# Kernel optimization log

Measured on AMD Instinct MI355X. Metric: run time of the kernel, lower is better.

## Reference

```python
import jax, jax.numpy as jnp
import numpy as np

TS = 0.01  # Euler step size (module's `ts`)

N_X, N_U, N_FEAT = 32, 16, 512
BATCH, SEQ_LEN = 512, 2048


def setup_inputs() -> dict:
    key = jax.random.key(0)
    k0, k1, k2, k3 = jax.random.split(key, 4)
    x0_batch = jax.random.normal(k0, (BATCH, 1, N_X), dtype=jnp.float32)
    u_batch = jax.random.normal(k1, (BATCH, SEQ_LEN, N_U), dtype=jnp.float32)
    # 2-layer MLP state-space model: Linear(n_x+n_u, n_feat) -> Tanh -> Linear(n_feat, n_x)
    fan1 = N_X + N_U
    W1 = jax.random.normal(k2, (fan1, N_FEAT), dtype=jnp.float32) / np.sqrt(fan1).astype(np.float32)
    b1 = jnp.zeros((N_FEAT,), dtype=jnp.float32)
    W2 = jax.random.normal(k3, (N_FEAT, N_X), dtype=jnp.float32) / np.sqrt(N_FEAT).astype(np.float32)
    b2 = jnp.zeros((N_X,), dtype=jnp.float32)
    return {"x0_batch": x0_batch, "u_batch": u_batch, "W1": W1, "b1": b1, "W2": W2, "b2": b2}


def reference(x0_batch, u_batch, W1, b1, W2, b2):
    # x0_batch: (B, 1, n_x); u_batch: (B, T, n_u) -> out: (B, T, n_x)
    x0 = x0_batch[:, 0, :]                       # (B, n_x)
    u_t = jnp.swapaxes(u_batch, 0, 1)            # (T, B, n_u) for scan over time

    def step(x, u):
        h = jnp.tanh(jnp.concatenate([x, u], axis=-1) @ W1 + b1)  # (B, n_feat)
        dx = h @ W2 + b2                                           # (B, n_x)
        x_next = x + TS * dx
        return x_next, x_next

    _, xs = jax.lax.scan(step, x0, u_t)          # xs: (T, B, n_x)
    return jnp.swapaxes(xs, 0, 1)                # (B, T, n_x)
```

## Files before the change

### kernel.cpp

```cpp
#include <hip/hip_runtime.h>

constexpr int NX = 32, NU = 16, NF = 512;
constexpr int SEQ = 2048;
constexpr int CH = 32;
constexpr int NT = 256;
constexpr float SC = 2.88539008177792681f;

template<int CTRL>
__device__ __forceinline__ float dpp_add(float v) {
    int t = __builtin_amdgcn_update_dpp(0, __float_as_int(v), CTRL, 0xF, 0xF, true);
    return v + __int_as_float(t);
}

__device__ __forceinline__ float tanh4(float y) {
    const float e = __builtin_amdgcn_exp2f(y);
    const float r = __builtin_amdgcn_rcpf(e + 1.f);
    return fmaf(-2.f, r, 1.f);
}

__global__ __launch_bounds__(NT, 2)
void fes_kernel(const float* __restrict__ x0, const float* __restrict__ ug,
                const float* __restrict__ W1, const float* __restrict__ b1,
                const float* __restrict__ W2, const float* __restrict__ b2,
                float* __restrict__ out)
{
    __shared__ float4 xs4[NX / 4];
    __shared__ float4 hs4[NF / 4];
    __shared__ float4 us4[CH * NU / 4];

    const int tid = threadIdx.x, row = blockIdx.x;
    const int g   = tid >> 1, kh = tid & 1;
    const int sl  = tid >> 4, l  = tid & 15;
    const int j0  = sl, j1 = sl + 16;

    float w1r[96];
#pragma unroll
    for (int i = 0; i < 24; ++i)
#pragma unroll
        for (int c = 0; c < 4; ++c)
            w1r[i * 4 + c] = SC * W1[(kh * 24 + i) * NF + 4 * g + c];
    float b1s[4];
#pragma unroll
    for (int c = 0; c < 4; ++c) b1s[c] = kh ? 0.f : SC * b1[4 * g + c];

    float w2a[32], w2b[32];
#pragma unroll
    for (int i = 0; i < 8; ++i)
#pragma unroll
        for (int c = 0; c < 4; ++c) {
            const int f = 4 * (l + 16 * i) + c;
            w2a[4 * i + c] = 0.01f * W2[f * NX + j0];
            w2b[4 * i + c] = 0.01f * W2[f * NX + j1];
        }
    const float bb0 = 0.01f * b2[j0], bb1 = 0.01f * b2[j1];

    float xr0 = x0[row * NX + j0];
    float xr1 = x0[row * NX + j1];

    const float* ug_row  = ug  + (size_t)row * SEQ * NU;
    float*       out_row = out + (size_t)row * SEQ * NX;

    if (tid < NX / 4) xs4[tid] = ((const float4*)(x0 + row * NX))[tid];

    const float4* bA = kh ? xs4 + 6 : xs4;

    for (int t0 = 0; t0 < SEQ; t0 += CH) {
        if (tid < CH * NU / 4)
            us4[tid] = *(const float4*)&ug_row[(size_t)t0 * NU + tid * 4];
        __syncthreads();

#pragma unroll 1
        for (int tc = 0; tc < CH; ++tc) {
            const int t = t0 + tc;
            const float4* bB = kh ? us4 + tc * 4 - 2 : xs4;
            const float4 iv0 = bA[0], iv1 = bA[1];
            const float4 iv2 = bB[2], iv3 = bB[3], iv4 = bB[4], iv5 = bB[5];
            float a0 = b1s[0], a1 = b1s[1], a2 = b1s[2], a3 = b1s[3];
#define G1F4(iv, q)                                                        \
            a0 = fmaf(w1r[(q)*16 + 0],  iv.x, a0);                         \
            a1 = fmaf(w1r[(q)*16 + 1],  iv.x, a1);                         \
            a2 = fmaf(w1r[(q)*16 + 2],  iv.x, a2);                         \
            a3 = fmaf(w1r[(q)*16 + 3],  iv.x, a3);                         \
            a0 = fmaf(w1r[(q)*16 + 4],  iv.y, a0);                         \
            a1 = fmaf(w1r[(q)*16 + 5],  iv.y, a1);                         \
            a2 = fmaf(w1r[(q)*16 + 6],  iv.y, a2);                         \
            a3 = fmaf(w1r[(q)*16 + 7],  iv.y, a3);                         \
            a0 = fmaf(w1r[(q)*16 + 8],  iv.z, a0);                         \
            a1 = fmaf(w1r[(q)*16 + 9],  iv.z, a1);                         \
            a2 = fmaf(w1r[(q)*16 + 10], iv.z, a2);                         \
            a3 = fmaf(w1r[(q)*16 + 11], iv.z, a3);                         \
            a0 = fmaf(w1r[(q)*16 + 12], iv.w, a0);                         \
            a1 = fmaf(w1r[(q)*16 + 13], iv.w, a1);                         \
            a2 = fmaf(w1r[(q)*16 + 14], iv.w, a2);                         \
            a3 = fmaf(w1r[(q)*16 + 15], iv.w, a3);
            G1F4(iv0, 0) G1F4(iv1, 1) G1F4(iv2, 2)
            G1F4(iv3, 3) G1F4(iv4, 4) G1F4(iv5, 5)
#undef G1F4
            a0 = dpp_add<0xB1>(a0);
            a1 = dpp_add<0xB1>(a1);
            a2 = dpp_add<0xB1>(a2);
            a3 = dpp_add<0xB1>(a3);
            float2 hw;
            hw.x = tanh4(kh ? a2 : a0);
            hw.y = tanh4(kh ? a3 : a1);
            ((float2*)hs4)[g * 2 + kh] = hw;
            __syncthreads();

            float sa0 = 0.f, sa1 = 0.f, sa2 = 0.f, sa3 = 0.f;
            float sb0 = 0.f, sb1 = 0.f, sb2 = 0.f, sb3 = 0.f;
#pragma unroll
            for (int i = 0; i < 8; ++i) {
                const float4 hv = hs4[l + 16 * i];
                sa0 = fmaf(hv.x, w2a[4*i],   sa0);
                sa1 = fmaf(hv.y, w2a[4*i+1], sa1);
                sa2 = fmaf(hv.z, w2a[4*i+2], sa2);
                sa3 = fmaf(hv.w, w2a[4*i+3], sa3);
                sb0 = fmaf(hv.x, w2b[4*i],   sb0);
                sb1 = fmaf(hv.y, w2b[4*i+1], sb1);
                sb2 = fmaf(hv.z, w2b[4*i+2], sb2);
                sb3 = fmaf(hv.w, w2b[4*i+3], sb3);
            }
            float sa = (sa0 + sa1) + (sa2 + sa3);
            float sb = (sb0 + sb1) + (sb2 + sb3);
            sa = dpp_add<0xB1>(sa);   sb = dpp_add<0xB1>(sb);
            sa = dpp_add<0x4E>(sa);   sb = dpp_add<0x4E>(sb);
            sa = dpp_add<0x124>(sa);  sb = dpp_add<0x124>(sb);
            sa = dpp_add<0x128>(sa);  sb = dpp_add<0x128>(sb);

            const float xn0 = xr0 + (sa + bb0);
            const float xn1 = xr1 + (sb + bb1);
            xr0 = xn0; xr1 = xn1;
            if (l < 2) {
                const float v  = l ? xn1 : xn0;
                const int   jj = j0 + (l << 4);
                ((float*)xs4)[jj] = v;
                out_row[(size_t)t * NX + jj] = v;
            }
            __syncthreads();
        }
    }
}

extern "C" void kernel_launch(void* const* d_in, const int* in_sizes, int n_in,
                              void* d_out, int out_size, void* d_ws, size_t ws_size,
                              hipStream_t stream) {
    const float* x0 = (const float*)d_in[0];
    const float* ug = (const float*)d_in[1];
    const float* W1 = (const float*)d_in[2];
    const float* b1 = (const float*)d_in[3];
    const float* W2 = (const float*)d_in[4];
    const float* b2 = (const float*)d_in[5];
    float* out = (float*)d_out;

    fes_kernel<<<dim3(512), dim3(NT), 0, stream>>>(x0, ug, W1, b1, W2, b2, out);
}
```

Baseline: 1.747 ms.

## Use packed FMA and reorganize output-stage reduction across 32-lane groups

Both matvecs are rewritten to use two-wide packed FP32 FMAs (v2f), which may compile to v_pk_fma_f32 and halve FMA instruction count. The second-layer work is remapped so each 32-lane half-wave reduces four output states over 512 features via a five-step DPP tree. One owner lane then writes a float4 to shared memory and global output instead of two scalar stores. This raises register use for packed weights and lengthens the reduction chain, at the risk of extra latency on the serial critical path.

```diff
diff --git a/kernel.cpp b/kernel.cpp
--- a/kernel.cpp
+++ b/kernel.cpp
@@ -1,4 +1,6 @@
 #include <hip/hip_runtime.h>
+
+typedef float v2f __attribute__((ext_vector_type(2)));
 
 constexpr int NX = 32, NU = 16, NF = 512;
 constexpr int SEQ = 2048;
@@ -18,6 +20,8 @@
     return fmaf(-2.f, r, 1.f);
 }
 
+__device__ __forceinline__ v2f pkfma(v2f a, v2f b, v2f c) { return a * b + c; }
+
 __global__ __launch_bounds__(NT, 2)
 void fes_kernel(const float* __restrict__ x0, const float* __restrict__ ug,
                 const float* __restrict__ W1, const float* __restrict__ b1,
@@ -29,33 +33,39 @@
     __shared__ float4 us4[CH * NU / 4];
 
     const int tid = threadIdx.x, row = blockIdx.x;
-    const int g   = tid >> 1, kh = tid & 1;
-    const int sl  = tid >> 4, l  = tid & 15;
-    const int j0  = sl, j1 = sl + 16;
+    const int lam = tid & 63, w = tid >> 6;
+    const int g = tid >> 1, kh = tid & 1;
+    const int sk = (lam & 15) | (((lam >> 4) & 1) << 4);
+    const int os = ((lam >> 5) & 1) + 2 * w;
+    const bool owner = (lam & 31) == 31;
 
-    float w1r[96];
+    v2f wk[48];
 #pragma unroll
-    for (int i = 0; i < 24; ++i)
+    for (int i = 0; i < 4; ++i)
 #pragma unroll
-        for (int c = 0; c < 4; ++c)
-            w1r[i * 4 + c] = SC * W1[(kh * 24 + i) * NF + 4 * g + c];
-    float b1s[4];
+        for (int kp = 0; kp < 12; ++kp) {
+            const int k = 24 * kh + 2 * kp;
+            wk[i * 12 + kp] = v2f{SC * W1[k * NF + 4 * g + i],
+                                  SC * W1[(k + 1) * NF + 4 * g + i]};
+        }
+    const float b1e = SC * b1[4 * g + 2 * kh];
+    const float b1o = SC * b1[4 * g + 2 * kh + 1];
+
+    v2f wc[4][8];
 #pragma unroll
-    for (int c = 0; c < 4; ++c) b1s[c] = kh ? 0.f : SC * b1[4 * g + c];
-
-    float w2a[32], w2b[32];
+    for (int c = 0; c < 4; ++c)
 #pragma unroll
-    for (int i = 0; i < 8; ++i)
+        for (int m = 0; m < 4; ++m)
 #pragma unroll
-        for (int c = 0; c < 4; ++c) {
-            const int f = 4 * (l + 16 * i) + c;
-            w2a[4 * i + c] = 0.01f * W2[f * NX + j0];
-            w2b[4 * i + c] = 0.01f * W2[f * NX + j1];
-        }
-    const float bb0 = 0.01f * b2[j0], bb1 = 0.01f * b2[j1];
-
-    float xr0 = x0[row * NX + j0];
-    float xr1 = x0[row * NX + j1];
+            for (int p = 0; p < 2; ++p) {
+                const int k = 128 * m + 4 * sk + 2 * p;
+                wc[c][2 * m + p] = v2f{0.01f * W2[k * NX + 4 * os + c],
+                                       0.01f * W2[(k + 1) * NX + 4 * os + c]};
+            }
+    float bb0 = 0.01f * b2[4 * os + 0], bb1 = 0.01f * b2[4 * os + 1];
+    float bb2 = 0.01f * b2[4 * os + 2], bb3 = 0.01f * b2[4 * os + 3];
+    float xr0 = x0[row * NX + 4 * os + 0], xr1 = x0[row * NX + 4 * os + 1];
+    float xr2 = x0[row * NX + 4 * os + 2], xr3 = x0[row * NX + 4 * os + 3];
 
     const float* ug_row  = ug  + (size_t)row * SEQ * NU;
     float*       out_row = out + (size_t)row * SEQ * NX;
@@ -63,6 +73,7 @@
     if (tid < NX / 4) xs4[tid] = ((const float4*)(x0 + row * NX))[tid];
 
     const float4* bA = kh ? xs4 + 6 : xs4;
+    const float4* hp = hs4 + sk;
 
     for (int t0 = 0; t0 < SEQ; t0 += CH) {
         if (tid < CH * NU / 4)
@@ -72,69 +83,69 @@
 #pragma unroll 1
         for (int tc = 0; tc < CH; ++tc) {
             const int t = t0 + tc;
-            const float4* bB = kh ? us4 + tc * 4 - 2 : xs4;
+            const float4* bB = kh ? us4 + 4 * tc - 2 : xs4;
             const float4 iv0 = bA[0], iv1 = bA[1];
             const float4 iv2 = bB[2], iv3 = bB[3], iv4 = bB[4], iv5 = bB[5];
-            float a0 = b1s[0], a1 = b1s[1], a2 = b1s[2], a3 = b1s[3];
-#define G1F4(iv, q)                                                        \
-            a0 = fmaf(w1r[(q)*16 + 0],  iv.x, a0);                         \
-            a1 = fmaf(w1r[(q)*16 + 1],  iv.x, a1);                         \
-            a2 = fmaf(w1r[(q)*16 + 2],  iv.x, a2);                         \
-            a3 = fmaf(w1r[(q)*16 + 3],  iv.x, a3);                         \
-            a0 = fmaf(w1r[(q)*16 + 4],  iv.y, a0);                         \
-            a1 = fmaf(w1r[(q)*16 + 5],  iv.y, a1);                         \
-            a2 = fmaf(w1r[(q)*16 + 6],  iv.y, a2);                         \
-            a3 = fmaf(w1r[(q)*16 + 7],  iv.y, a3);                         \
-            a0 = fmaf(w1r[(q)*16 + 8],  iv.z, a0);                         \
-            a1 = fmaf(w1r[(q)*16 + 9],  iv.z, a1);                         \
-            a2 = fmaf(w1r[(q)*16 + 10], iv.z, a2);                         \
-            a3 = fmaf(w1r[(q)*16 + 11], iv.z, a3);                         \
-            a0 = fmaf(w1r[(q)*16 + 12], iv.w, a0);                         \
-            a1 = fmaf(w1r[(q)*16 + 13], iv.w, a1);                         \
-            a2 = fmaf(w1r[(q)*16 + 14], iv.w, a2);                         \
-            a3 = fmaf(w1r[(q)*16 + 15], iv.w, a3);
-            G1F4(iv0, 0) G1F4(iv1, 1) G1F4(iv2, 2)
-            G1F4(iv3, 3) G1F4(iv4, 4) G1F4(iv5, 5)
-#undef G1F4
-            a0 = dpp_add<0xB1>(a0);
-            a1 = dpp_add<0xB1>(a1);
-            a2 = dpp_add<0xB1>(a2);
-            a3 = dpp_add<0xB1>(a3);
+            v2f a0 = {0.f, 0.f}, a1 = {0.f, 0.f}, a2 = {0.f, 0.f}, a3 = {0.f, 0.f};
+#define G1S(iv, s)                                                          \
+            {   const v2f lo = {iv.x, iv.y}, hi = {iv.z, iv.w};             \
+                a0 = pkfma(wk[0*12 + 2*(s)], lo, a0);                       \
+                a1 = pkfma(wk[1*12 + 2*(s)], lo, a1);                       \
+                a2 = pkfma(wk[2*12 + 2*(s)], lo, a2);                       \
+                a3 = pkfma(wk[3*12 + 2*(s)], lo, a3);                       \
+                a0 = pkfma(wk[0*12 + 2*(s) + 1], hi, a0);                   \
+                a1 = pkfma(wk[1*12 + 2*(s) + 1], hi, a1);                   \
+                a2 = pkfma(wk[2*12 + 2*(s) + 1], hi, a2);                   \
+                a3 = pkfma(wk[3*12 + 2*(s) + 1], hi, a3); }
+            G1S(iv0, 0) G1S(iv1, 1) G1S(iv2, 2) G1S(iv3, 3) G1S(iv4, 4) G1S(iv5, 5)
+#undef G1S
+            float h0 = a0.x + a0.y, h1 = a1.x + a1.y;
+            float h2 = a2.x + a2.y, h3 = a3.x + a3.y;
+            h0 = dpp_add<0xB1>(h0);  h1 = dpp_add<0xB1>(h1);
+            h2 = dpp_add<0xB1>(h2);  h3 = dpp_add<0xB1>(h3);
+            const float he = kh ? h2 : h0, ho = kh ? h3 : h1;
             float2 hw;
-            hw.x = tanh4(kh ? a2 : a0);
-            hw.y = tanh4(kh ? a3 : a1);
-            ((float2*)hs4)[g * 2 + kh] = hw;
+            hw.x = tanh4(he + b1e);
+            hw.y = tanh4(ho + b1o);
+            ((float2*)hs4)[2 * g + kh] = hw;
             __syncthreads();
 
-            float sa0 = 0.f, sa1 = 0.f, sa2 = 0.f, sa3 = 0.f;
-            float sb0 = 0.f, sb1 = 0.f, sb2 = 0.f, sb3 = 0.f;
+            v2f A0 = {0.f, 0.f}, A1 = {0.f, 0.f}, A2 = {0.f, 0.f}, A3 = {0.f, 0.f};
 #pragma unroll
-            for (int i = 0; i < 8; ++i) {
-                const float4 hv = hs4[l + 16 * i];
-                sa0 = fmaf(hv.x, w2a[4*i],   sa0);
-                sa1 = fmaf(hv.y, w2a[4*i+1], sa1);
-                sa2 = fmaf(hv.z, w2a[4*i+2], sa2);
-                sa3 = fmaf(hv.w, w2a[4*i+3], sa3);
-                sb0 = fmaf(hv.x, w2b[4*i],   sb0);
-                sb1 = fmaf(hv.y, w2b[4*i+1], sb1);
-                sb2 = fmaf(hv.z, w2b[4*i+2], sb2);
-                sb3 = fmaf(hv.w, w2b[4*i+3], sb3);
+            for (int m = 0; m < 4; ++m) {
+                const float4 hv = hp[32 * m];
+                const v2f lo = {hv.x, hv.y}, hi = {hv.z, hv.w};
+                A0 = pkfma(wc[0][2 * m], lo, A0);
+                A1 = pkfma(wc[1][2 * m], lo, A1);
+                A2 = pkfma(wc[2][2 * m], lo, A2);
+                A3 = pkfma(wc[3][2 * m], lo, A3);
+                A0 = pkfma(wc[0][2 * m + 1], hi, A0);
+                A1 = pkfma(wc[1][2 * m + 1], hi, A1);
+                A2 = pkfma(wc[2][2 * m + 1], hi, A2);
+                A3 = pkfma(wc[3][2 * m + 1], hi, A3);
             }
-            float sa = (sa0 + sa1) + (sa2 + sa3);
-            float sb = (sb0 + sb1) + (sb2 + sb3);
-            sa = dpp_add<0xB1>(sa);   sb = dpp_add<0xB1>(sb);
-            sa = dpp_add<0x4E>(sa);   sb = dpp_add<0x4E>(sb);
-            sa = dpp_add<0x124>(sa);  sb = dpp_add<0x124>(sb);
-            sa = dpp_add<0x128>(sa);  sb = dpp_add<0x128>(sb);
+            float s0 = A0.x + A0.y, s1 = A1.x + A1.y;
+            float s2 = A2.x + A2.y, s3 = A3.x + A3.y;
+            s0 = dpp_add<0xB1>(s0);  s1 = dpp_add<0xB1>(s1);
+            s2 = dpp_add<0xB1>(s2);  s3 = dpp_add<0xB1>(s3);
+            s0 = dpp_add<0x4E>(s0);  s1 = dpp_add<0x4E>(s1);
+            s2 = dpp_add<0x4E>(s2);  s3 = dpp_add<0x4E>(s3);
+            s0 = dpp_add<0x124>(s0); s1 = dpp_add<0x124>(s1);
+            s2 = dpp_add<0x124>(s2); s3 = dpp_add<0x124>(s3);
+            s0 = dpp_add<0x128>(s0); s1 = dpp_add<0x128>(s1);
+            s2 = dpp_add<0x128>(s2); s3 = dpp_add<0x128>(s3);
+            s0 = dpp_add<0x142>(s0); s1 = dpp_add<0x142>(s1);
+            s2 = dpp_add<0x142>(s2); s3 = dpp_add<0x142>(s3);
 
-            const float xn0 = xr0 + (sa + bb0);
-            const float xn1 = xr1 + (sb + bb1);
-            xr0 = xn0; xr1 = xn1;
-            if (l < 2) {
-                const float v  = l ? xn1 : xn0;
-                const int   jj = j0 + (l << 4);
-                ((float*)xs4)[jj] = v;
-                out_row[(size_t)t * NX + jj] = v;
+            const float xn0 = xr0 + (s0 + bb0);
+            const float xn1 = xr1 + (s1 + bb1);
+            const float xn2 = xr2 + (s2 + bb2);
+            const float xn3 = xr3 + (s3 + bb3);
+            xr0 = xn0; xr1 = xn1; xr2 = xn2; xr3 = xn3;
+            if (owner) {
+                const float4 xv = {xn0, xn1, xn2, xn3};
+                xs4[os] = xv;
+                *(float4*)&out_row[(size_t)t * NX + 4 * os] = xv;
             }
             __syncthreads();
         }
```

New measurement: 1.719 ms. Within noise of the previous version (-1.6%).
